# Kernel tuning notes

Measured on AMD Instinct MI355X. Metric: run time of the kernel, lower is better.

## Reference

```python
import jax, jax.numpy as jnp
import numpy as np
import math

N_HEAD = 16
N_KV_HEAD = 4
HEAD_DIM = 128
ROTARY_DIM = 128
ROTARY_BASE = 10000
N_CTX = 2048


def _sin_cos(rotary_dim, n_ctx, base):
    pos = np.arange(n_ctx, dtype=np.float32)
    dim = np.arange(rotary_dim // 2, dtype=np.float32)
    freq = base ** (dim / (rotary_dim / 2))
    freq = np.concatenate([freq, freq])  # non-adjacent-pairs layout
    angles = pos[:, None] / freq[None, :]
    return jnp.asarray(np.sin(angles)), jnp.asarray(np.cos(angles))


def _rotate_half(x):
    n = x.shape[-1] // 2
    return jnp.concatenate([-x[..., n:], x[..., :n]], axis=-1)


def setup_inputs() -> dict:
    key = jax.random.key(0)
    ks = jax.random.split(key, 5)
    B, T, C = 2, 2048, 2048
    kv = N_KV_HEAD * HEAD_DIM
    s = 0.02
    return {
        "x": jax.random.normal(ks[0], (B, T, C), jnp.float32),
        "Wq": jax.random.normal(ks[1], (C, C), jnp.float32) * s,
        "Wk": jax.random.normal(ks[2], (kv, C), jnp.float32) * s,
        "Wv": jax.random.normal(ks[3], (kv, C), jnp.float32) * s,
        "Wo": jax.random.normal(ks[4], (C, C), jnp.float32) * s,
    }


def reference(x, Wq, Wk, Wv, Wo):
    B, T, C = x.shape
    q = (x @ Wq.T).reshape(B, T, N_HEAD, HEAD_DIM).transpose(0, 2, 1, 3)    # bhtd
    k = (x @ Wk.T).reshape(B, T, N_KV_HEAD, HEAD_DIM).transpose(0, 2, 1, 3)
    v = (x @ Wv.T).reshape(B, T, N_KV_HEAD, HEAD_DIM).transpose(0, 2, 1, 3)

    sin, cos = _sin_cos(ROTARY_DIM, N_CTX, ROTARY_BASE)
    pos = jnp.arange(T)
    c = cos[pos][None, None, :, :]  # 1,1,T,rot
    s = sin[pos][None, None, :, :]
    q = q * c + _rotate_half(q) * s
    k = k * c + _rotate_half(k) * s

    rep = N_HEAD // N_KV_HEAD
    k = jnp.repeat(k, rep, axis=1)
    v = jnp.repeat(v, rep, axis=1)

    scale = 1.0 / math.sqrt(HEAD_DIM)
    att = jnp.einsum("bhqd,bhkd->bhqk", q, k) * scale
    causal = jnp.tril(jnp.ones((T, T), bool))
    att = jnp.where(causal[None, None], att, -jnp.inf)
    att = jax.nn.softmax(att, axis=-1)
    y = jnp.einsum("bhqk,bhkd->bhqd", att, v)
    y = y.transpose(0, 2, 1, 3).reshape(B, T, C)
    return y @ Wo.T
```

## Files before the change

kernel.cpp:

```cpp
#include <hip/hip_runtime.h>
#include <hip/hip_bf16.h>

typedef float f32x4 __attribute__((ext_vector_type(4)));
typedef float f32x16 __attribute__((ext_vector_type(16)));
typedef short s16x8 __attribute__((ext_vector_type(8)));
typedef short s16x4 __attribute__((ext_vector_type(4)));

__device__ __forceinline__ short f2bf(float f) {
  union { float f; unsigned u; } v; v.f = f;
  unsigned r = v.u + 0x7fffu + ((v.u >> 16) & 1u);
  return (short)(r >> 16);
}
__device__ __forceinline__ float bf2f(short s) {
  union { unsigned u; float f; } v; v.u = ((unsigned)(unsigned short)s) << 16;
  return v.f;
}
__device__ __forceinline__ unsigned cvtpk(float lo, float hi) {
  unsigned r;
  asm("v_cvt_pk_bf16_f32 %0, %1, %2" : "=v"(r) : "v"(lo), "v"(hi));
  return r;
}

__device__ __forceinline__ void gload_lds16(const short* g, short* l) {
  __builtin_amdgcn_global_load_lds(
      (const __attribute__((address_space(1))) void*)g,
      (__attribute__((address_space(3))) void*)l, 16, 0, 0);
}

__global__ __launch_bounds__(256) void k_f2bf(const float* __restrict__ in,
                                              short* __restrict__ out, int n8) {
  int i = blockIdx.x * 256 + threadIdx.x;
  if (i >= n8) return;
  const float4* p = (const float4*)in + (size_t)i * 2;
  float4 a = p[0], b = p[1];
  s16x8 o;
  o[0] = f2bf(a.x); o[1] = f2bf(a.y); o[2] = f2bf(a.z); o[3] = f2bf(a.w);
  o[4] = f2bf(b.x); o[5] = f2bf(b.y); o[6] = f2bf(b.z); o[7] = f2bf(b.w);
  *(s16x8*)(out + (size_t)i * 8) = o;
}

__global__ __launch_bounds__(256) void k_f2bfw(const float* __restrict__ s0,
                                               const float* __restrict__ s1,
                                               const float* __restrict__ s2,
                                               const float* __restrict__ s3,
                                               short* __restrict__ dqkv,
                                               short* __restrict__ dwo) {
  int i = blockIdx.x * 256 + threadIdx.x;
  const float* src;
  short* dst;
  if (i < 524288) { src = s0 + (size_t)i * 8; dst = dqkv + (size_t)i * 8; }
  else if (i < 655360) { int j = i - 524288; src = s1 + (size_t)j * 8; dst = dqkv + 4194304 + (size_t)j * 8; }
  else if (i < 786432) { int j = i - 655360; src = s2 + (size_t)j * 8; dst = dqkv + 5242880 + (size_t)j * 8; }
  else { int j = i - 786432; src = s3 + (size_t)j * 8; dst = dwo + (size_t)j * 8; }
  const float4* p = (const float4*)src;
  float4 a = p[0], b = p[1];
  s16x8 o;
  o[0] = f2bf(a.x); o[1] = f2bf(a.y); o[2] = f2bf(a.z); o[3] = f2bf(a.w);
  o[4] = f2bf(b.x); o[5] = f2bf(b.y); o[6] = f2bf(b.z); o[7] = f2bf(b.w);
  *(s16x8*)dst = o;
}

template <int MODE>
__global__ __launch_bounds__(256) void k_gemm_bt(const short* __restrict__ A,
                                                 const short* __restrict__ Bw,
                                                 void* __restrict__ C,
                                                 void* __restrict__ C2,
                                                 void* __restrict__ C3,
                                                 int M, int N, int K) {
  __shared__ __align__(16) short As[128 * 64];
  __shared__ __align__(16) short Bs[128 * 64];
  const int tid = threadIdx.x;
  const int w = tid >> 6, lane = tid & 63;
  const int wm = w >> 1, wn = w & 1;
  const int nbx = gridDim.x;
  const int f = blockIdx.y * nbx + blockIdx.x;
  const int cpx = (nbx * gridDim.y) >> 3;
  const int sw = (f & 7) * cpx + (f >> 3);
  const int bm = sw / nbx, bn = sw % nbx;
  const int l15 = lane & 15, l4 = lane >> 4;

  f32x4 acc[4][4] = {};

  const int nk = K >> 6;
  for (int kt = 0; kt < nk; ++kt) {
    __syncthreads();
#pragma unroll
    for (int it = 0; it < 4; ++it) {
      int p = it * 256 + tid;
      int p0 = it * 256 + w * 64;
      int r = p >> 3, j = p & 7;
      int jsrc = j ^ (r & 7);
      gload_lds16(A + (size_t)(bm * 128 + r) * K + kt * 64 + jsrc * 8, &As[p0 * 8]);
      gload_lds16(Bw + (size_t)(bn * 128 + r) * K + kt * 64 + jsrc * 8, &Bs[p0 * 8]);
    }
    __syncthreads();
#pragma unroll
    for (int kk = 0; kk < 2; ++kk) {
      s16x8 af[4], bf[4];
      const int jj = kk * 4 + l4;
#pragma unroll
      for (int mi = 0; mi < 4; ++mi) {
        int r = wm * 64 + mi * 16 + l15;
        af[mi] = *(const s16x8*)&As[(r * 8 + (jj ^ (r & 7))) * 8];
      }
#pragma unroll
      for (int ni = 0; ni < 4; ++ni) {
        int r = wn * 64 + ni * 16 + l15;
        bf[ni] = *(const s16x8*)&Bs[(r * 8 + (jj ^ (r & 7))) * 8];
      }
      __builtin_amdgcn_s_setprio(1);
#pragma unroll
      for (int mi = 0; mi < 4; ++mi)
#pragma unroll
        for (int ni = 0; ni < 4; ++ni)
          acc[mi][ni] = __builtin_amdgcn_mfma_f32_16x16x32_bf16(
              af[mi], bf[ni], acc[mi][ni], 0, 0, 0);
      __builtin_amdgcn_s_setprio(0);
    }
  }

#pragma unroll
  for (int mi = 0; mi < 4; ++mi) {
#pragma unroll
    for (int ni = 0; ni < 4; ++ni) {
      int row0 = bm * 128 + wm * 64 + mi * 16 + l4 * 4;
      int col = bn * 128 + wn * 64 + ni * 16 + l15;
      if (MODE == 1) {
        float* Cf = (float*)C;
#pragma unroll
        for (int r2 = 0; r2 < 4; ++r2)
          Cf[(size_t)(row0 + r2) * N + col] = acc[mi][ni][r2];
      } else {
        if (col < 2048) {
          short* Qo = (short*)C;
#pragma unroll
          for (int r2 = 0; r2 < 4; ++r2)
            Qo[(size_t)(row0 + r2) * 2048 + col] = f2bf(acc[mi][ni][r2]);
        } else if (col < 2560) {
          short* Ko = (short*)C2;
#pragma unroll
          for (int r2 = 0; r2 < 4; ++r2)
            Ko[(size_t)(row0 + r2) * 512 + (col - 2048)] = f2bf(acc[mi][ni][r2]);
        } else {
          short* Vo = (short*)C3;
          int b = row0 >> 11, t0 = row0 & 2047;
          s16x4 pk;
#pragma unroll
          for (int r2 = 0; r2 < 4; ++r2) pk[r2] = f2bf(acc[mi][ni][r2]);
          *(s16x4*)&Vo[(size_t)b * 1048576 + (size_t)(col - 2560) * 2048 + t0] = pk;
        }
      }
    }
  }
}

__global__ __launch_bounds__(256) void k_rope(short* __restrict__ X, int shift,
                                              int rowstride, float mul) {
  int idx = blockIdx.x * 256 + threadIdx.x;
  int row = idx >> shift;
  int rem = idx & ((1 << shift) - 1);
  int h = rem >> 6, d = rem & 63;
  int t = row & 2047;
  float inv = exp2f(-(float)d * (13.287712379549449f / 64.f));
  float ang = (float)t * inv;
  float s, c;
  sincosf(ang, &s, &c);
  size_t base = (size_t)row * rowstride + h * 128 + d;
  float q0 = bf2f(X[base]), q1 = bf2f(X[base + 64]);
  X[base] = f2bf((q0 * c - q1 * s) * mul);
  X[base + 64] = f2bf((q1 * c + q0 * s) * mul);
}

__global__ void k_zero(int* p) { if (threadIdx.x == 0) *p = 0; }

__global__ __launch_bounds__(256, 2) void k_attn5(const short* __restrict__ Q,
                                                  const short* __restrict__ Kb,
                                                  const short* __restrict__ Vt,
                                                  short* __restrict__ Y,
                                                  int* __restrict__ qcnt) {
  __shared__ __align__(16) short Ks[2][64 * 128];
  __shared__ __align__(16) float mgb[2][4352];
  __shared__ int s_item;

  const int tid = threadIdx.x;
  const int w = tid >> 6, lane = tid & 63;
  const int l31 = lane & 31, h5 = lane >> 5;
  const int qc0 = (w >> 1) << 5;
  const int par = w & 1;

  for (;;) {
    if (tid == 0) s_item = atomicAdd(qcnt, 1);
    __syncthreads();
    const int item = s_item;
    if (item >= 1024) return;
    const int qi = 31 - (item >> 5);
    const int h = (item >> 1) & 15;
    const int b = item & 1;
    const int kh = h >> 2;
    const int q0 = qi << 6;

    s16x8 qf[8];
    const size_t qrow = (size_t)(b * 2048 + q0 + qc0 + l31);
#pragma unroll
    for (int f = 0; f < 8; ++f)
      qf[f] = *(const s16x8*)(Q + qrow * 2048 + h * 128 + f * 16 + h5 * 8);

    {
      const float tpos = (float)(q0 + qc0 + l31);
#pragma unroll
      for (int f = 0; f < 4; ++f) {
#pragma unroll
        for (int e = 0; e < 8; ++e) {
          int d = f * 16 + h5 * 8 + e;
          float inv = exp2f((float)d * (-13.287712379549449f / 64.f));
          float sn, cs;
          __sincosf(tpos * inv, &sn, &cs);
          float a = bf2f(qf[f][e]), bv = bf2f(qf[f + 4][e]);
          qf[f][e]     = f2bf((a * cs - bv * sn) * 0.12751758912141852f);
          qf[f + 4][e] = f2bf((bv * cs + a * sn) * 0.12751758912141852f);
        }
      }
    }

    f32x16 oacc[4] = {};
    float m = -1e30f, l = 0.f;

    auto stage = [&](int buf, int t) {
#pragma unroll
      for (int it = 0; it < 4; ++it) {
        int p = it * 256 + tid;
        int p0 = it * 256 + w * 64;
        int r = p >> 4, c = p & 15;
        int csrc = (c - r) & 15;
        gload_lds16(Kb + (size_t)(b * 2048 + t * 64 + r) * 512 + kh * 128 + csrc * 8,
                    &Ks[buf][p0 * 8]);
      }
    };

    stage(0, 0);
    __syncthreads();

    const short* Vb = Vt + (size_t)b * 1048576 + (size_t)(kh * 128) * 2048;

    for (int t = 0; t <= qi; ++t) {
      const int cur = t & 1;
      if (t < qi) stage(cur ^ 1, t + 1);

      const bool skipw = (t == qi) && (w == 1);
      if (!skipw) {
        f32x16 sa = {};
        const int kr = par * 32 + l31;
        __builtin_amdgcn_s_setprio(1);
#pragma unroll
        for (int f = 0; f < 8; ++f) {
          int c = f * 2 + h5;
          s16x8 kf = *(const s16x8*)&Ks[cur][(kr * 16 + ((c + kr) & 15)) * 8];
          sa = __builtin_amdgcn_mfma_f32_32x32x16_bf16(kf, qf[f], sa, 0, 0, 0);
        }
        __builtin_amdgcn_s_setprio(0);

        s16x8 vf[4][2];
#pragma unroll
        for (int dblk = 0; dblk < 4; ++dblk)
#pragma unroll
          for (int kk = 0; kk < 2; ++kk) {
            int r = dblk * 32 + l31;
            int c = par * 4 + kk * 2 + h5;
            vf[dblk][kk] = *(const s16x8*)(Vb + (size_t)r * 2048 + t * 64 + c * 8);
          }

        if (t == qi && (w == 0 || w == 3)) {
#pragma unroll
          for (int rg = 0; rg < 16; ++rg) {
            int krow = (rg & 3) + 8 * (rg >> 2) + 4 * h5;
            if (krow > l31) sa[rg] = -3.0e38f;
          }
        }

        float mx[16];
#pragma unroll
        for (int i = 0; i < 16; ++i) mx[i] = sa[i];
#pragma unroll
        for (int stp = 8; stp > 0; stp >>= 1)
#pragma unroll
          for (int i = 0; i < stp; ++i) mx[i] = fmaxf(mx[i], mx[i + stp]);
        float pm = fmaxf(mx[0], __shfl_xor(mx[0], 32));

        if (!__all(pm - m <= 8.f)) {
          float mn = fmaxf(m, pm);
          float al = exp2f(m - mn);
          m = mn;
          l *= al;
#pragma unroll
          for (int d = 0; d < 4; ++d)
#pragma unroll
            for (int i = 0; i < 16; ++i) oacc[d][i] *= al;
        }

        float sm[16];
#pragma unroll
        for (int i = 0; i < 16; ++i) {
          float e = exp2f(sa[i] - m);
          sa[i] = e;
          sm[i] = e;
        }
#pragma unroll
        for (int stp = 8; stp > 0; stp >>= 1)
#pragma unroll
          for (int i = 0; i < stp; ++i) sm[i] += sm[i + stp];
        l += sm[0] + __shfl_xor(sm[0], 32);

        unsigned u[8], pu[8];
#pragma unroll
        for (int g = 0; g < 4; ++g) {
          u[2 * g]     = cvtpk(sa[4 * g + 0], sa[4 * g + 1]);
          u[2 * g + 1] = cvtpk(sa[4 * g + 2], sa[4 * g + 3]);
        }
#pragma unroll
        for (int g2 = 0; g2 < 8; ++g2) pu[g2] = __shfl_xor(u[g2], 32);
        s16x8 pb[2];
#pragma unroll
        for (int kk = 0; kk < 2; ++kk) {
          union { unsigned uu[4]; s16x8 v; } cv;
          cv.uu[0] = h5 ? pu[4 * kk + 2] : u[4 * kk];
          cv.uu[1] = h5 ? pu[4 * kk + 3] : u[4 * kk + 1];
          cv.uu[2] = h5 ? u[4 * kk + 2]  : pu[4 * kk];
          cv.uu[3] = h5 ? u[4 * kk + 3]  : pu[4 * kk + 1];
          pb[kk] = cv.v;
        }

        __builtin_amdgcn_s_setprio(1);
#pragma unroll
        for (int dblk = 0; dblk < 4; ++dblk)
#pragma unroll
          for (int kk = 0; kk < 2; ++kk)
            oacc[dblk] = __builtin_amdgcn_mfma_f32_32x32x16_bf16(
                vf[dblk][kk], pb[kk], oacc[dblk], 0, 0, 0);
        __builtin_amdgcn_s_setprio(0);
      }

      __syncthreads();
    }

    const int base = (h5 * 32 + l31) * 68;
    if (par) {
      float* mg = &mgb[w >> 1][0];
#pragma unroll
      for (int d = 0; d < 4; ++d)
#pragma unroll
        for (int rg = 0; rg < 4; ++rg) {
          f32x4 tv;
          tv[0] = oacc[d][rg * 4 + 0];
          tv[1] = oacc[d][rg * 4 + 1];
          tv[2] = oacc[d][rg * 4 + 2];
          tv[3] = oacc[d][rg * 4 + 3];
          *(f32x4*)&mg[base + d * 16 + rg * 4] = tv;
        }
      mg[base + 64] = m;
      mg[base + 65] = l;
    }
    __syncthreads();
    if (!par) {
      const float* mg = &mgb[w >> 1][0];
      float m1 = mg[base + 64], l1 = mg[base + 65];
      float ms = fmaxf(m, m1);
      float a0 = exp2f(m - ms), a1 = exp2f(m1 - ms);
      float li = 1.f / (l * a0 + l1 * a1);
#pragma unroll
      for (int d = 0; d < 4; ++d) {
#pragma unroll
        for (int rg = 0; rg < 4; ++rg) {
          f32x4 po = *(const f32x4*)&mg[base + d * 16 + rg * 4];
          float v0 = (oacc[d][rg * 4 + 0] * a0 + po[0] * a1) * li;
          float v1 = (oacc[d][rg * 4 + 1] * a0 + po[1] * a1) * li;
          float v2 = (oacc[d][rg * 4 + 2] * a0 + po[2] * a1) * li;
          float v3 = (oacc[d][rg * 4 + 3] * a0 + po[3] * a1) * li;
          uint2 st;
          st.x = cvtpk(v0, v1);
          st.y = cvtpk(v2, v3);
          int d0 = d * 32 + 8 * rg + 4 * h5;
          *(uint2*)(Y + qrow * 2048 + h * 128 + d0) = st;
        }
      }
    }
  }
}

extern "C" void kernel_launch(void* const* d_in, const int* in_sizes, int n_in,
                              void* d_out, int out_size, void* d_ws, size_t ws_size,
                              hipStream_t stream) {
  (void)in_sizes; (void)n_in; (void)out_size; (void)ws_size;
  const float* x  = (const float*)d_in[0];
  const float* Wq = (const float*)d_in[1];
  const float* Wk = (const float*)d_in[2];
  const float* Wv = (const float*)d_in[3];
  const float* Wo = (const float*)d_in[4];

  char* ws = (char*)d_ws;
  short* xb    = (short*)(ws);
  short* wqkvb = (short*)(ws + 16777216);
  short* wob   = (short*)(ws + 29360128);
  short* Qb    = (short*)(ws + 37748736);
  short* Kb    = (short*)(ws + 54525952);
  short* Vtb   = (short*)(ws + 58720256);
  short* Yb    = (short*)(ws + 62914560);
  int* qcnt    = (int*)(ws + 29360128 - 64);

  k_f2bf<<<4096, 256, 0, stream>>>(x, xb, 1048576);
  k_f2bfw<<<5120, 256, 0, stream>>>(Wq, Wk, Wv, Wo, wqkvb, wob);

  k_gemm_bt<3><<<dim3(24, 32), 256, 0, stream>>>(xb, wqkvb, Qb, Kb, Vtb,
                                                 4096, 3072, 2048);

  k_rope<<<4096, 256, 0, stream>>>(Kb, 8, 512, 1.0f);

  k_zero<<<1, 64, 0, stream>>>(qcnt);
  k_attn5<<<512, 256, 0, stream>>>(Qb, Kb, Vtb, Yb, qcnt);

  k_gemm_bt<1><<<dim3(16, 32), 256, 0, stream>>>(Yb, wob, d_out, nullptr,
                                                 nullptr, 4096, 2048, 2048);
}
```

Baseline: 213.5 us.

## Load K fragments directly from global memory instead of staging through LDS

The attention kernel stops double-buffering K tiles in shared memory with async global-to-LDS loads. Each wave now reads its K fragments straight from global memory into registers, the same way V was already read. This removes the per-iteration block barrier and the LDS traffic. In exchange, K is read redundantly by waves that share rows, and global load latency is no longer hidden by prefetching the next tile.

```diff
diff --git a/kernel.cpp b/kernel.cpp
--- a/kernel.cpp
+++ b/kernel.cpp
@@ -173,12 +173,11 @@
 
 __global__ void k_zero(int* p) { if (threadIdx.x == 0) *p = 0; }
 
-__global__ __launch_bounds__(256, 2) void k_attn5(const short* __restrict__ Q,
+__global__ __launch_bounds__(256, 2) void k_attn6(const short* __restrict__ Q,
                                                   const short* __restrict__ Kb,
                                                   const short* __restrict__ Vt,
                                                   short* __restrict__ Y,
                                                   int* __restrict__ qcnt) {
-  __shared__ __align__(16) short Ks[2][64 * 128];
   __shared__ __align__(16) float mgb[2][4352];
   __shared__ int s_item;
 
@@ -187,6 +186,7 @@
   const int l31 = lane & 31, h5 = lane >> 5;
   const int qc0 = (w >> 1) << 5;
   const int par = w & 1;
+  const int kr = par * 32 + l31;
 
   for (;;) {
     if (tid == 0) s_item = atomicAdd(qcnt, 1);
@@ -225,39 +225,16 @@
     f32x16 oacc[4] = {};
     float m = -1e30f, l = 0.f;
 
-    auto stage = [&](int buf, int t) {
-#pragma unroll
-      for (int it = 0; it < 4; ++it) {
-        int p = it * 256 + tid;
-        int p0 = it * 256 + w * 64;
-        int r = p >> 4, c = p & 15;
-        int csrc = (c - r) & 15;
-        gload_lds16(Kb + (size_t)(b * 2048 + t * 64 + r) * 512 + kh * 128 + csrc * 8,
-                    &Ks[buf][p0 * 8]);
-      }
-    };
-
-    stage(0, 0);
-    __syncthreads();
-
+    const short* Kbase = Kb + (size_t)(b * 2048 + kr) * 512 + kh * 128 + h5 * 8;
     const short* Vb = Vt + (size_t)b * 1048576 + (size_t)(kh * 128) * 2048;
 
     for (int t = 0; t <= qi; ++t) {
-      const int cur = t & 1;
-      if (t < qi) stage(cur ^ 1, t + 1);
-
       const bool skipw = (t == qi) && (w == 1);
       if (!skipw) {
-        f32x16 sa = {};
-        const int kr = par * 32 + l31;
-        __builtin_amdgcn_s_setprio(1);
-#pragma unroll
-        for (int f = 0; f < 8; ++f) {
-          int c = f * 2 + h5;
-          s16x8 kf = *(const s16x8*)&Ks[cur][(kr * 16 + ((c + kr) & 15)) * 8];
-          sa = __builtin_amdgcn_mfma_f32_32x32x16_bf16(kf, qf[f], sa, 0, 0, 0);
-        }
-        __builtin_amdgcn_s_setprio(0);
+        s16x8 kf[8];
+#pragma unroll
+        for (int f = 0; f < 8; ++f)
+          kf[f] = *(const s16x8*)(Kbase + (size_t)t * 64 * 512 + f * 16);
 
         s16x8 vf[4][2];
 #pragma unroll
@@ -268,6 +245,13 @@
             int c = par * 4 + kk * 2 + h5;
             vf[dblk][kk] = *(const s16x8*)(Vb + (size_t)r * 2048 + t * 64 + c * 8);
           }
+
+        f32x16 sa = {};
+        __builtin_amdgcn_s_setprio(1);
+#pragma unroll
+        for (int f = 0; f < 8; ++f)
+          sa = __builtin_amdgcn_mfma_f32_32x32x16_bf16(kf[f], qf[f], sa, 0, 0, 0);
+        __builtin_amdgcn_s_setprio(0);
 
         if (t == qi && (w == 0 || w == 3)) {
 #pragma unroll
@@ -338,8 +322,6 @@
                 vf[dblk][kk], pb[kk], oacc[dblk], 0, 0, 0);
         __builtin_amdgcn_s_setprio(0);
       }
-
-      __syncthreads();
     }
 
     const int base = (h5 * 32 + l31) * 68;
@@ -415,7 +397,7 @@
   k_rope<<<4096, 256, 0, stream>>>(Kb, 8, 512, 1.0f);
 
   k_zero<<<1, 64, 0, stream>>>(qcnt);
-  k_attn5<<<512, 256, 0, stream>>>(Qb, Kb, Vtb, Yb, qcnt);
+  k_attn6<<<512, 256, 0, stream>>>(Qb, Kb, Vtb, Yb, qcnt);
 
   k_gemm_bt<1><<<dim3(16, 32), 256, 0, stream>>>(Yb, wob, d_out, nullptr,
                                                  nullptr, 4096, 2048, 2048);
```

After: 252.5 us. 1.18x slower.

## Stage V tiles into LDS via async double-buffered loads in attention

Applied to the files above, without the earlier changes.

The attention kernel now prefetches V tiles into a swizzled, double-buffered LDS region with global_load_lds, alongside the K tiles, instead of reading V fragments directly from global memory. K and V fragments are read from LDS into registers before the next tile's asynchronous load is issued. The softmax merge scratch buffer is aliased onto the K/V LDS buffers to keep the LDS footprint roughly unchanged. The aim is to hide global V latency behind compute, at the cost of more registers held live across the loop and extra LDS traffic.

```diff
diff --git a/kernel.cpp b/kernel.cpp
--- a/kernel.cpp
+++ b/kernel.cpp
@@ -173,13 +173,13 @@
 
 __global__ void k_zero(int* p) { if (threadIdx.x == 0) *p = 0; }
 
-__global__ __launch_bounds__(256, 2) void k_attn5(const short* __restrict__ Q,
+__global__ __launch_bounds__(256, 2) void k_attn7(const short* __restrict__ Q,
                                                   const short* __restrict__ Kb,
                                                   const short* __restrict__ Vt,
                                                   short* __restrict__ Y,
                                                   int* __restrict__ qcnt) {
   __shared__ __align__(16) short Ks[2][64 * 128];
-  __shared__ __align__(16) float mgb[2][4352];
+  __shared__ __align__(16) short Vs[2][128 * 64];
   __shared__ int s_item;
 
   const int tid = threadIdx.x;
@@ -235,39 +235,53 @@
         gload_lds16(Kb + (size_t)(b * 2048 + t * 64 + r) * 512 + kh * 128 + csrc * 8,
                     &Ks[buf][p0 * 8]);
       }
+#pragma unroll
+      for (int it = 0; it < 4; ++it) {
+        int p = it * 256 + tid;
+        int p0 = it * 256 + w * 64;
+        int r = p >> 3, c = p & 7;
+        int csrc = (c - r) & 7;
+        gload_lds16(Vt + (size_t)b * 1048576 + (size_t)(kh * 128 + r) * 2048 +
+                        t * 64 + csrc * 8,
+                    &Vs[buf][p0 * 8]);
+      }
     };
 
     stage(0, 0);
     __syncthreads();
 
-    const short* Vb = Vt + (size_t)b * 1048576 + (size_t)(kh * 128) * 2048;
-
     for (int t = 0; t <= qi; ++t) {
       const int cur = t & 1;
-      if (t < qi) stage(cur ^ 1, t + 1);
-
       const bool skipw = (t == qi) && (w == 1);
+
+      s16x8 kf[8];
+      s16x8 vf[4][2];
       if (!skipw) {
-        f32x16 sa = {};
         const int kr = par * 32 + l31;
-        __builtin_amdgcn_s_setprio(1);
 #pragma unroll
         for (int f = 0; f < 8; ++f) {
           int c = f * 2 + h5;
-          s16x8 kf = *(const s16x8*)&Ks[cur][(kr * 16 + ((c + kr) & 15)) * 8];
-          sa = __builtin_amdgcn_mfma_f32_32x32x16_bf16(kf, qf[f], sa, 0, 0, 0);
-        }
-        __builtin_amdgcn_s_setprio(0);
-
-        s16x8 vf[4][2];
+          kf[f] = *(const s16x8*)&Ks[cur][(kr * 16 + ((c + kr) & 15)) * 8];
+        }
 #pragma unroll
         for (int dblk = 0; dblk < 4; ++dblk)
 #pragma unroll
           for (int kk = 0; kk < 2; ++kk) {
             int r = dblk * 32 + l31;
             int c = par * 4 + kk * 2 + h5;
-            vf[dblk][kk] = *(const s16x8*)(Vb + (size_t)r * 2048 + t * 64 + c * 8);
+            vf[dblk][kk] = *(const s16x8*)&Vs[cur][(r * 8 + ((c + r) & 7)) * 8];
           }
+      }
+
+      if (t < qi) stage(cur ^ 1, t + 1);
+
+      if (!skipw) {
+        f32x16 sa = {};
+        __builtin_amdgcn_s_setprio(1);
+#pragma unroll
+        for (int f = 0; f < 8; ++f)
+          sa = __builtin_amdgcn_mfma_f32_32x32x16_bf16(kf[f], qf[f], sa, 0, 0, 0);
+        __builtin_amdgcn_s_setprio(0);
 
         if (t == qi && (w == 0 || w == 3)) {
 #pragma unroll
@@ -344,7 +358,7 @@
 
     const int base = (h5 * 32 + l31) * 68;
     if (par) {
-      float* mg = &mgb[w >> 1][0];
+      float* mg = (w == 1) ? (float*)&Ks[0][0] : (float*)&Vs[0][0];
 #pragma unroll
       for (int d = 0; d < 4; ++d)
 #pragma unroll
@@ -361,7 +375,7 @@
     }
     __syncthreads();
     if (!par) {
-      const float* mg = &mgb[w >> 1][0];
+      const float* mg = (w == 0) ? (const float*)&Ks[0][0] : (const float*)&Vs[0][0];
       float m1 = mg[base + 64], l1 = mg[base + 65];
       float ms = fmaxf(m, m1);
       float a0 = exp2f(m - ms), a1 = exp2f(m1 - ms);
@@ -415,7 +429,7 @@
   k_rope<<<4096, 256, 0, stream>>>(Kb, 8, 512, 1.0f);
 
   k_zero<<<1, 64, 0, stream>>>(qcnt);
-  k_attn5<<<512, 256, 0, stream>>>(Qb, Kb, Vtb, Yb, qcnt);
+  k_attn7<<<512, 256, 0, stream>>>(Qb, Kb, Vtb, Yb, qcnt);
 
   k_gemm_bt<1><<<dim3(16, 32), 256, 0, stream>>>(Yb, wob, d_out, nullptr,
                                                  nullptr, 4096, 2048, 2048);
```

Measured after the change: 210.5 us. Within noise of the previous version (-1.4%).

## Stage V tiles through LDS with register prefetch and reuse K buffers for merge

Applied to the files above, without the earlier changes.

The attention kernel now loads each V tile cooperatively into registers one iteration ahead, writes it to a swizzled LDS buffer after the barrier, and reads the MFMA operands from LDS. Before, every wave fetched its own V fragments straight from global memory. The K double buffer, the V buffer and the final merge scratch now share one 48KB LDS region, which lowers LDS use so the launch bounds drop the min-blocks hint and the persistent grid grows from 512 to 768 blocks. In exchange there is an extra barrier per iteration and more register pressure from the prefetch.

```diff
diff --git a/kernel.cpp b/kernel.cpp
--- a/kernel.cpp
+++ b/kernel.cpp
@@ -173,20 +173,26 @@
 
 __global__ void k_zero(int* p) { if (threadIdx.x == 0) *p = 0; }
 
-__global__ __launch_bounds__(256, 2) void k_attn5(const short* __restrict__ Q,
-                                                  const short* __restrict__ Kb,
-                                                  const short* __restrict__ Vt,
-                                                  short* __restrict__ Y,
-                                                  int* __restrict__ qcnt) {
-  __shared__ __align__(16) short Ks[2][64 * 128];
-  __shared__ __align__(16) float mgb[2][4352];
+__global__ __launch_bounds__(256) void k_attn8(const short* __restrict__ Q,
+                                               const short* __restrict__ Kb,
+                                               const short* __restrict__ Vt,
+                                               short* __restrict__ Y,
+                                               int* __restrict__ qcnt) {
+  __shared__ __align__(16) char smem[49152];
   __shared__ int s_item;
+  short* Ks0 = (short*)smem;
+  short* Ks1 = (short*)(smem + 16384);
+  short* Vs  = (short*)(smem + 32768);
+  float* mg0 = (float*)smem;
+  float* mg1 = (float*)(smem + 17408);
 
   const int tid = threadIdx.x;
   const int w = tid >> 6, lane = tid & 63;
   const int l31 = lane & 31, h5 = lane >> 5;
   const int qc0 = (w >> 1) << 5;
   const int par = w & 1;
+  const int vr0 = tid >> 3, vc0 = tid & 7;
+  const int vslot = (vc0 + vr0) & 7;
 
   for (;;) {
     if (tid == 0) s_item = atomicAdd(qcnt, 1);
@@ -225,7 +231,7 @@
     f32x16 oacc[4] = {};
     float m = -1e30f, l = 0.f;
 
-    auto stage = [&](int buf, int t) {
+    auto stageK = [&](short* buf, int t) {
 #pragma unroll
       for (int it = 0; it < 4; ++it) {
         int p = it * 256 + tid;
@@ -233,18 +239,37 @@
         int r = p >> 4, c = p & 15;
         int csrc = (c - r) & 15;
         gload_lds16(Kb + (size_t)(b * 2048 + t * 64 + r) * 512 + kh * 128 + csrc * 8,
-                    &Ks[buf][p0 * 8]);
+                    &buf[p0 * 8]);
       }
     };
 
-    stage(0, 0);
-    __syncthreads();
-
-    const short* Vb = Vt + (size_t)b * 1048576 + (size_t)(kh * 128) * 2048;
+    uint4 vreg[4];
+    auto vload = [&](int t) {
+#pragma unroll
+      for (int q = 0; q < 4; ++q) {
+        int r = q * 32 + vr0;
+        vreg[q] = *(const uint4*)(Vt + (size_t)b * 1048576 +
+                                  (size_t)(kh * 128 + r) * 2048 + t * 64 + vc0 * 8);
+      }
+    };
+    auto vwrite = [&]() {
+#pragma unroll
+      for (int q = 0; q < 4; ++q) {
+        int r = q * 32 + vr0;
+        *(uint4*)&Vs[(r * 8 + vslot) * 8] = vreg[q];
+      }
+    };
+
+    stageK(Ks0, 0);
+    vload(0);
+    __syncthreads();
+    vwrite();
+    __syncthreads();
 
     for (int t = 0; t <= qi; ++t) {
-      const int cur = t & 1;
-      if (t < qi) stage(cur ^ 1, t + 1);
+      short* Kcur = (t & 1) ? Ks1 : Ks0;
+      short* Knxt = (t & 1) ? Ks0 : Ks1;
+      if (t < qi) { stageK(Knxt, t + 1); vload(t + 1); }
 
       const bool skipw = (t == qi) && (w == 1);
       if (!skipw) {
@@ -254,20 +279,10 @@
 #pragma unroll
         for (int f = 0; f < 8; ++f) {
           int c = f * 2 + h5;
-          s16x8 kf = *(const s16x8*)&Ks[cur][(kr * 16 + ((c + kr) & 15)) * 8];
+          s16x8 kf = *(const s16x8*)&Kcur[(kr * 16 + ((c + kr) & 15)) * 8];
           sa = __builtin_amdgcn_mfma_f32_32x32x16_bf16(kf, qf[f], sa, 0, 0, 0);
         }
         __builtin_amdgcn_s_setprio(0);
-
-        s16x8 vf[4][2];
-#pragma unroll
-        for (int dblk = 0; dblk < 4; ++dblk)
-#pragma unroll
-          for (int kk = 0; kk < 2; ++kk) {
-            int r = dblk * 32 + l31;
-            int c = par * 4 + kk * 2 + h5;
-            vf[dblk][kk] = *(const s16x8*)(Vb + (size_t)r * 2048 + t * 64 + c * 8);
-          }
 
         if (t == qi && (w == 0 || w == 3)) {
 #pragma unroll
@@ -333,18 +348,26 @@
 #pragma unroll
         for (int dblk = 0; dblk < 4; ++dblk)
 #pragma unroll
-          for (int kk = 0; kk < 2; ++kk)
+          for (int kk = 0; kk < 2; ++kk) {
+            int r = dblk * 32 + l31;
+            int c = par * 4 + kk * 2 + h5;
+            s16x8 vfr = *(const s16x8*)&Vs[(r * 8 + ((c + r) & 7)) * 8];
             oacc[dblk] = __builtin_amdgcn_mfma_f32_32x32x16_bf16(
-                vf[dblk][kk], pb[kk], oacc[dblk], 0, 0, 0);
+                vfr, pb[kk], oacc[dblk], 0, 0, 0);
+          }
         __builtin_amdgcn_s_setprio(0);
       }
 
       __syncthreads();
+      if (t < qi) {
+        vwrite();
+        __syncthreads();
+      }
     }
 
     const int base = (h5 * 32 + l31) * 68;
     if (par) {
-      float* mg = &mgb[w >> 1][0];
+      float* mg = (w == 1) ? mg0 : mg1;
 #pragma unroll
       for (int d = 0; d < 4; ++d)
 #pragma unroll
@@ -361,7 +384,7 @@
     }
     __syncthreads();
     if (!par) {
-      const float* mg = &mgb[w >> 1][0];
+      const float* mg = (w == 0) ? mg0 : mg1;
       float m1 = mg[base + 64], l1 = mg[base + 65];
       float ms = fmaxf(m, m1);
       float a0 = exp2f(m - ms), a1 = exp2f(m1 - ms);
@@ -415,7 +438,7 @@
   k_rope<<<4096, 256, 0, stream>>>(Kb, 8, 512, 1.0f);
 
   k_zero<<<1, 64, 0, stream>>>(qcnt);
-  k_attn5<<<512, 256, 0, stream>>>(Qb, Kb, Vtb, Yb, qcnt);
+  k_attn8<<<768, 256, 0, stream>>>(Qb, Kb, Vtb, Yb, qcnt);
 
   k_gemm_bt<1><<<dim3(16, 32), 256, 0, stream>>>(Yb, wob, d_out, nullptr,
                                                  nullptr, 4096, 2048, 2048);
```

New measurement: 290.6 us. 1.36x slower.
